# Kernel optimization log

Measured on AMD Instinct MI355X. Metric: run time of the kernel, lower is better.

The kernel has to match this reference:

```python
import jax, jax.numpy as jnp
import numpy as np

N_ROUTES = 200000
N_REGIONS = 2048
D_IN = 3
EMBED_DIM0 = 100
LSTM_DIM = 100
H1 = 1000
D_OUT = 100


def setup_inputs() -> dict:
    key = jax.random.key(0)
    ks = jax.random.split(key, 14)
    s = 0.1
    return {
        "routes_last": jax.random.normal(ks[0], (N_ROUTES, D_IN), jnp.float32),
        "route_region_ids": jax.random.randint(ks[1], (N_ROUTES,), 0, N_REGIONS),
        # linear0: Linear(3, 100)
        "W0": jax.random.normal(ks[2], (EMBED_DIM0, D_IN), jnp.float32) * s,
        "b0": jax.random.normal(ks[3], (EMBED_DIM0,), jnp.float32) * s,
        # LSTMCell(100, 100): gate order i, f, g, o
        "Wih": jax.random.normal(ks[4], (4 * LSTM_DIM, EMBED_DIM0), jnp.float32) * s,
        "bih": jax.random.normal(ks[5], (4 * LSTM_DIM,), jnp.float32) * s,
        "Whh": jax.random.normal(ks[6], (4 * LSTM_DIM, LSTM_DIM), jnp.float32) * s,
        "bhh": jax.random.normal(ks[7], (4 * LSTM_DIM,), jnp.float32) * s,
        # learned initial state (nn.Parameter rand(1, lstm_dim))
        "h0": jax.random.uniform(ks[8], (1, LSTM_DIM), jnp.float32),
        "c0": jax.random.uniform(ks[9], (1, LSTM_DIM), jnp.float32),
        # linears1: Linear(100,1000) -> ReLU -> Linear(1000,100)
        "W1": jax.random.normal(ks[10], (H1, LSTM_DIM), jnp.float32) * s,
        "b1": jax.random.normal(ks[11], (H1,), jnp.float32) * s,
        "W2": jax.random.normal(ks[12], (D_OUT, H1), jnp.float32) * s,
        "b2": jax.random.normal(ks[13], (D_OUT,), jnp.float32) * s,
        "num_regions": N_REGIONS,
    }


def reference(routes_last, route_region_ids, W0, b0, Wih, bih, Whh, bhh, h0, c0, W1, b1, W2, b2, num_regions):
    # Note: the original LSTM loop always restarts from (h0, c0) and keeps only the
    # last hx, so only the last timestep of each route matters. routes_last is that point.
    e = routes_last @ W0.T + b0                       # [N, 100]
    gates = e @ Wih.T + bih + (h0 @ Whh.T + bhh)      # [N, 400]; h0 broadcasts
    i_g, f_g, g_g, o_g = jnp.split(gates, 4, axis=-1)
    c = jax.nn.sigmoid(f_g) * c0 + jax.nn.sigmoid(i_g) * jnp.tanh(g_g)
    h = jax.nn.sigmoid(o_g) * jnp.tanh(c)             # [N, 100]
    hx = jax.nn.relu(h @ W1.T + b1) @ W2.T + b2       # [N, 100]
    # sum routes within each region (ragged sum)
    region_emb = jax.ops.segment_sum(hx, route_region_ids, num_segments=num_regions)  # [R, 100]
    region_emb = region_emb / jnp.linalg.norm(region_emb, axis=-1, keepdims=True)
    cov = region_emb @ region_emb.T                   # [R, R] cosine similarity
    idx = jnp.arange(num_regions)
    cov = cov.at[idx, idx].set(-jnp.inf)
    return cov
```

## Files before the change

### kernel.cpp

```cpp
#include <hip/hip_runtime.h>
#include <math.h>

#define NR 200000
#define NREG 2048
#define BR 128
#define NBLK 1563

typedef short bf16x8 __attribute__((ext_vector_type(8)));
typedef float f32x4 __attribute__((ext_vector_type(4)));

#define SH_WIH 410752
#define SH_W1  (SH_WIH + 57344)
#define SH_W2  (SH_W1 + 131072)
#define B_LIST 1427712
#define B_CNT  2227712
#define B_BASE 2235904
#define B_CURS 2244112
#define B_HXB  2252800
#define WS_REQ 91852800ULL

#define L_SA  0
#define L_SB  16384
#define L_HB  30720
#define L_T1  63488
#define L_B1C 79872
#define L_RID 80128
#define L_BYTES 80640
#define A_XS  (L_T1)
#define A_GBP (L_T1 + 1536)
#define A_C0P (L_T1 + 3328)

__device__ __forceinline__ unsigned f2bf(float f) {
    unsigned u = __builtin_bit_cast(unsigned, f);
    u += 0x7fff + ((u >> 16) & 1);
    return u >> 16;
}
__device__ __forceinline__ float sigm(float x) { return 1.0f / (1.0f + __expf(-x)); }
__device__ __forceinline__ float tanhfast(float x) {
    float t = __expf(2.0f * fabsf(x));
    float r = 1.0f - 2.0f / (t + 1.0f);
    return copysignf(r, x);
}
__device__ __forceinline__ f32x4 mfma16(bf16x8 a, bf16x8 b, f32x4 c) {
    return __builtin_amdgcn_mfma_f32_16x16x32_bf16(a, b, c, 0, 0, 0);
}

__global__ __launch_bounds__(1024) void k_zero(float* __restrict__ p, int n) {
    int i = blockIdx.x * 1024 + threadIdx.x;
    if (i < n) p[i] = 0.0f;
}

__global__ __launch_bounds__(256) void k_hist(const int* __restrict__ ids,
                                              int* __restrict__ cnt) {
    int i = blockIdx.x * 256 + threadIdx.x;
    if (i < NR) atomicAdd(&cnt[ids[i]], 1);
}

__global__ __launch_bounds__(1024) void k_scan(const int* __restrict__ cnt,
                                               int* __restrict__ base,
                                               int* __restrict__ cursor) {
    __shared__ int sc[2048];
    const int t = threadIdx.x;
    sc[t] = cnt[t];
    sc[t + 1024] = cnt[t + 1024];
    __syncthreads();
    for (int off = 1; off < 2048; off <<= 1) {
        int v0 = (t >= off) ? sc[t - off] : 0;
        int v1 = sc[t + 1024 - off];
        __syncthreads();
        sc[t] += v0;
        sc[t + 1024] += v1;
        __syncthreads();
    }
    int b0 = (t == 0) ? 0 : sc[t - 1];
    int b1v = sc[t + 1023];
    base[t] = b0;          cursor[t] = b0;
    base[t + 1024] = b1v;  cursor[t + 1024] = b1v;
    if (t == 0) base[2048] = sc[2047];
}

__global__ __launch_bounds__(256) void k_scatter(const int* __restrict__ ids,
                                                 int* __restrict__ cursor,
                                                 int* __restrict__ list) {
    int i = blockIdx.x * 256 + threadIdx.x;
    if (i < NR) {
        int pos = atomicAdd(&cursor[ids[i]], 1);
        list[pos] = i;
    }
}

__global__ __launch_bounds__(256) void k_prep(
    const float* __restrict__ Wih, const float* __restrict__ bih,
    const float* __restrict__ bhh, const float* __restrict__ Whh,
    const float* __restrict__ h0,  const float* __restrict__ c0,
    const float* __restrict__ W1,  const float* __restrict__ W2,
    float* __restrict__ wsf, short* __restrict__ wsh)
{
    int idx = blockIdx.x * 256 + threadIdx.x;
    if (idx < 57344) {
        int st = idx >> 13, s = idx & 8191;
        int row = s >> 7, c4 = (s >> 3) & 15, e = s & 7;
        int kc = c4 ^ (row & 15);
        int k = kc * 8 + e;
        int g = row >> 4, j = st * 16 + (row & 15);
        float v = (j < 100 && k < 100) ? Wih[(g * 100 + j) * 100 + k] : 0.f;
        wsh[SH_WIH + idx] = (short)f2bf(v);
        return;
    }
    idx -= 57344;
    if (idx < 131072) {
        int st = idx >> 13, s = idx & 8191;
        int row = s >> 7, c4 = (s >> 3) & 15, e = s & 7;
        int kc = c4 ^ (row & 15);
        int k = kc * 8 + e;
        int m = st * 64 + row;
        float v = (m < 1000 && k < 100) ? W1[m * 100 + k] : 0.f;
        wsh[SH_W1 + idx] = (short)f2bf(v);
        return;
    }
    idx -= 131072;
    if (idx < 114688) {
        int st = idx / 7168, s = idx - st * 7168;
        int row = s >> 6, c4 = (s >> 3) & 7, e = s & 7;
        int kc = c4 ^ (row & 7);
        int m = st * 64 + kc * 8 + e;
        float v = (row < 100 && m < 1000) ? W2[row * 1000 + m] : 0.f;
        wsh[SH_W2 + idx] = (short)f2bf(v);
        return;
    }
    idx -= 114688;
    if (idx < 448) {
        int jt = idx >> 6, r = idx & 63, g = r >> 4, j = jt * 16 + (r & 15);
        float s = 0.f;
        if (j < 100) {
            s = bih[g * 100 + j] + bhh[g * 100 + j];
            const float* wr = &Whh[(g * 100 + j) * 100];
            for (int k = 0; k < 100; ++k) s += h0[k] * wr[k];
        }
        wsf[204800 + idx] = s;
        return;
    }
    idx -= 448;
    if (idx < 112) wsf[205248 + idx] = (idx < 100) ? c0[idx] : 0.f;
}

__global__ __launch_bounds__(256, 2) void k_routes(
    const float* __restrict__ routes, const int* __restrict__ ids,
    const float* __restrict__ W0, const float* __restrict__ b0,
    const float* __restrict__ b1, const float* __restrict__ b2,
    const float* __restrict__ wsf, const short* __restrict__ wsh,
    float* __restrict__ racc, float* __restrict__ hxb, int use_hxb)
{
    __shared__ __align__(16) float ldsf[L_BYTES / 4];
    char* L = (char*)ldsf;
    const int tid = threadIdx.x;
    const int w = tid >> 6, l = tid & 63;
    const int lr = l & 15, lg = l >> 4;
    const int rbase = blockIdx.x * BR;

    float* xs  = (float*)(L + A_XS);
    float* gbp = (float*)(L + A_GBP);
    float* c0p = (float*)(L + A_C0P);
    float* b1c = (float*)(L + L_B1C);
    int*   rid = (int*)(L + L_RID);

    if (tid < 96) {
        float4 v;
        int gi = rbase * 3 + tid * 4;
        v.x = (gi + 0 < NR * 3) ? routes[gi + 0] : 0.f;
        v.y = (gi + 1 < NR * 3) ? routes[gi + 1] : 0.f;
        v.z = (gi + 2 < NR * 3) ? routes[gi + 2] : 0.f;
        v.w = (gi + 3 < NR * 3) ? routes[gi + 3] : 0.f;
        *(float4*)(xs + tid * 4) = v;
    } else if (tid >= 128) {
        int t = tid - 128;
        rid[t] = (rbase + t < NR) ? ids[rbase + t] : 0;
    }
    for (int i = tid; i < 448; i += 256) gbp[i] = wsf[204800 + i];
    for (int i = tid; i < 112; i += 256) c0p[i] = wsf[205248 + i];
    if (tid < 128) {
        int q = tid & 15;
        f32x4 z = {0.f, 0.f, 0.f, 0.f};
        *(f32x4*)(L + L_HB + tid * 256 + ((14 ^ q) << 4)) = z;
        *(f32x4*)(L + L_HB + tid * 256 + ((15 ^ q) << 4)) = z;
    }
    __syncthreads();

    bf16x8 be[2][4];
    #pragma unroll
    for (int rt = 0; rt < 2; ++rt) {
        int rl = w * 32 + rt * 16 + lr;
        float x0 = xs[rl * 3], x1 = xs[rl * 3 + 1], x2 = xs[rl * 3 + 2];
        #pragma unroll
        for (int ks = 0; ks < 4; ++ks) {
            bf16x8 v;
            #pragma unroll
            for (int j = 0; j < 8; ++j) {
                int k = ks * 32 + lg * 8 + j;
                float e = 0.f;
                if (k < 100)
                    e = b0[k] + x0 * W0[3 * k] + x1 * W0[3 * k + 1] + x2 * W0[3 * k + 2];
                v[j] = (short)f2bf(e);
            }
            be[rt][ks] = v;
        }
    }

    const f32x4* gsrc = (const f32x4*)(wsh + SH_WIH);
    f32x4 pa[4];
    #pragma unroll
    for (int t = 0; t < 4; ++t) pa[t] = gsrc[tid + t * 256];
    #pragma unroll 1
    for (int jt = 0; jt < 7; ++jt) {
        __syncthreads();
        {
            f32x4* dst = (f32x4*)(L + L_SA);
            #pragma unroll
            for (int t = 0; t < 4; ++t) dst[tid + t * 256] = pa[t];
        }
        __syncthreads();
        if (jt < 6) {
            #pragma unroll
            for (int t = 0; t < 4; ++t) pa[t] = gsrc[(jt + 1) * 1024 + tid + t * 256];
        }
        f32x4 acc[4][2];
        #pragma unroll
        for (int g = 0; g < 4; ++g) {
            bf16x8 aw[4];
            #pragma unroll
            for (int ks = 0; ks < 4; ++ks)
                aw[ks] = *(bf16x8*)(L + L_SA + (g * 16 + lr) * 256 + (((lg + 4 * ks) ^ lr) << 4));
            #pragma unroll
            for (int rt = 0; rt < 2; ++rt) {
                f32x4 a = {0.f, 0.f, 0.f, 0.f};
                #pragma unroll
                for (int ks = 0; ks < 4; ++ks) a = mfma16(aw[ks], be[rt][ks], a);
                acc[g][rt] = a;
            }
        }
        const f32x4 gi_ = *(const f32x4*)(gbp + jt * 64 +  0 + lg * 4);
        const f32x4 gf_ = *(const f32x4*)(gbp + jt * 64 + 16 + lg * 4);
        const f32x4 gg_ = *(const f32x4*)(gbp + jt * 64 + 32 + lg * 4);
        const f32x4 go_ = *(const f32x4*)(gbp + jt * 64 + 48 + lg * 4);
        const f32x4 c0v = *(const f32x4*)(c0p + jt * 16 + lg * 4);
        #pragma unroll
        for (int rt = 0; rt < 2; ++rt) {
            int route = w * 32 + rt * 16 + lr;
            short4 hs;
            #pragma unroll
            for (int i = 0; i < 4; ++i) {
                float iv = sigm(acc[0][rt][i] + gi_[i]);
                float fv = sigm(acc[1][rt][i] + gf_[i]);
                float gv = tanhfast(acc[2][rt][i] + gg_[i]);
                float ov = sigm(acc[3][rt][i] + go_[i]);
                float c  = fv * c0v[i] + iv * gv;
                float h  = ov * tanhfast(c);
                ((short*)&hs)[i] = (short)f2bf(h);
            }
            int c4 = 2 * jt + (lg >> 1);
            *(short4*)(L + L_HB + route * 256 + ((c4 ^ lr) << 4) + (lg & 1) * 8) = hs;
        }
    }

    bf16x8 bh[2][4];
    #pragma unroll
    for (int rt = 0; rt < 2; ++rt)
        #pragma unroll
        for (int ks = 0; ks < 4; ++ks)
            bh[rt][ks] = *(bf16x8*)(L + L_HB + (w * 32 + rt * 16 + lr) * 256 + (((lg + 4 * ks) ^ lr) << 4));

    const f32x4* s1 = (const f32x4*)(wsh + SH_W1);
    const f32x4* s2 = (const f32x4*)(wsh + SH_W2);
    f32x4 p1[4], p2[4];
    float pb1 = 0.f;
    #pragma unroll
    for (int t = 0; t < 4; ++t) p1[t] = s1[tid + t * 256];
    #pragma unroll
    for (int t = 0; t < 4; ++t) {
        int s = tid + t * 256;
        p2[t] = (s < 896) ? s2[s] : f32x4{0.f, 0.f, 0.f, 0.f};
    }
    if (tid < 64) pb1 = b1[tid];

    f32x4 hx[7][2] = {};
    #pragma unroll 1
    for (int mc = 0; mc < 16; ++mc) {
        __syncthreads();
        {
            f32x4* d1 = (f32x4*)(L + L_SA);
            #pragma unroll
            for (int t = 0; t < 4; ++t) d1[tid + t * 256] = p1[t];
            f32x4* d2 = (f32x4*)(L + L_SB);
            #pragma unroll
            for (int t = 0; t < 4; ++t) {
                int s = tid + t * 256;
                if (s < 896) d2[s] = p2[t];
            }
            if (tid < 64) b1c[tid] = pb1;
        }
        __syncthreads();
        if (mc < 15) {
            #pragma unroll
            for (int t = 0; t < 4; ++t) p1[t] = s1[(mc + 1) * 1024 + tid + t * 256];
            #pragma unroll
            for (int t = 0; t < 4; ++t) {
                int s = tid + t * 256;
                if (s < 896) p2[t] = s2[(mc + 1) * 896 + s];
            }
            if (tid < 64) {
                int m = (mc + 1) * 64 + tid;
                pb1 = (m < 1000) ? b1[m] : 0.f;
            }
        }
        #pragma unroll
        for (int mt = 0; mt < 4; ++mt) {
            bf16x8 aw[4];
            #pragma unroll
            for (int ks = 0; ks < 4; ++ks)
                aw[ks] = *(bf16x8*)(L + L_SA + (mt * 16 + lr) * 256 + (((lg + 4 * ks) ^ lr) << 4));
            const f32x4 b1v = *(const f32x4*)(b1c + mt * 16 + lg * 4);
            #pragma unroll
            for (int rt = 0; rt < 2; ++rt) {
                f32x4 a = {0.f, 0.f, 0.f, 0.f};
                #pragma unroll
                for (int ks = 0; ks < 4; ++ks) a = mfma16(aw[ks], bh[rt][ks], a);
                int route = w * 32 + rt * 16 + lr;
                short4 ts;
                #pragma unroll
                for (int i = 0; i < 4; ++i)
                    ((short*)&ts)[i] = (short)f2bf(fmaxf(a[i] + b1v[i], 0.f));
                int c4 = 2 * mt + (lg >> 1);
                *(short4*)(L + L_T1 + route * 128 + ((c4 ^ (lr & 7)) << 4) + (lg & 1) * 8) = ts;
            }
        }
        bf16x8 bt[2][2];
        #pragma unroll
        for (int rt = 0; rt < 2; ++rt)
            #pragma unroll
            for (int k2 = 0; k2 < 2; ++k2)
                bt[rt][k2] = *(bf16x8*)(L + L_T1 + (w * 32 + rt * 16 + lr) * 128 + (((4 * k2 + lg) ^ (lr & 7)) << 4));
        #pragma unroll
        for (int dt = 0; dt < 7; ++dt) {
            bf16x8 aw2[2];
            #pragma unroll
            for (int k2 = 0; k2 < 2; ++k2)
                aw2[k2] = *(bf16x8*)(L + L_SB + (dt * 16 + lr) * 128 + (((4 * k2 + lg) ^ (lr & 7)) << 4));
            #pragma unroll
            for (int rt = 0; rt < 2; ++rt)
                #pragma unroll
                for (int k2 = 0; k2 < 2; ++k2)
                    hx[dt][rt] = mfma16(aw2[k2], bt[rt][k2], hx[dt][rt]);
        }
    }

    if (use_hxb) {
        #pragma unroll
        for (int rt = 0; rt < 2; ++rt) {
            int rl = w * 32 + rt * 16 + lr;
            if (rbase + rl < NR) {
                float* dst = hxb + (rbase + rl) * 112;
                #pragma unroll
                for (int dt = 0; dt < 7; ++dt) {
                    int d0 = dt * 16 + lg * 4;
                    f32x4 v = hx[dt][rt];
                    #pragma unroll
                    for (int i = 0; i < 4; ++i)
                        v[i] += (d0 + i < 100) ? b2[d0 + i] : 0.f;
                    *(f32x4*)(dst + d0) = v;
                }
            }
        }
    } else {
        #pragma unroll
        for (int rt = 0; rt < 2; ++rt) {
            int rl = w * 32 + rt * 16 + lr;
            if (rbase + rl < NR) {
                float* dst = &racc[rid[rl] * 100];
                #pragma unroll
                for (int dt = 0; dt < 7; ++dt) {
                    int dbase = dt * 16 + lg * 4;
                    #pragma unroll
                    for (int i = 0; i < 4; ++i) {
                        int d = dbase + i;
                        if (d < 100) atomicAdd(&dst[d], hx[dt][rt][i] + b2[d]);
                    }
                }
            }
        }
    }
}

__global__ __launch_bounds__(128) void k_segsum(const int* __restrict__ base,
                                                const int* __restrict__ list,
                                                const float* __restrict__ hxb,
                                                float* __restrict__ racc) {
    __shared__ int ll[1024];
    __shared__ float pp[2];
    const int reg = blockIdx.x, t = threadIdx.x;
    const int s = base[reg], e = base[reg + 1];
    const int n = e - s;
    const int d = t;
    float acc = 0.f;
    if (n <= 1024) {
        for (int i = t; i < n; i += 128) ll[i] = list[s + i];
        __syncthreads();
        #pragma unroll 2
        for (int i = 0; i < n; ++i) {
            int rt = ll[i];
            if (d < 112) acc += hxb[rt * 112 + d];
        }
    } else {
        for (int i = 0; i < n; ++i) {
            int rt = list[s + i];
            if (d < 112) acc += hxb[rt * 112 + d];
        }
    }
    float sq = (d < 100) ? acc * acc : 0.f;
    #pragma unroll
    for (int o = 32; o; o >>= 1) sq += __shfl_xor(sq, o);
    if ((t & 63) == 0) pp[t >> 6] = sq;
    __syncthreads();
    float rn = 1.0f / sqrtf(pp[0] + pp[1]);
    if (d < 100) racc[reg * 100 + d] = acc * rn;
}

__global__ __launch_bounds__(64) void k_norm(float* __restrict__ E) {
    const int r = blockIdx.x;
    const int l = threadIdx.x;
    float v0 = E[r * 100 + l];
    float v1 = (l < 36) ? E[r * 100 + 64 + l] : 0.0f;
    float s = v0 * v0 + v1 * v1;
    #pragma unroll
    for (int o = 32; o; o >>= 1) s += __shfl_xor(s, o);
    const float rn = 1.0f / sqrtf(s);
    E[r * 100 + l] = v0 * rn;
    if (l < 36) E[r * 100 + 64 + l] = v1 * rn;
}

#define ST 68
__global__ __launch_bounds__(256) void k_cov(const float* __restrict__ E,
                                             float* __restrict__ out) {
    __shared__ float aT[100 * ST];
    __shared__ float bT[100 * ST];
    const int bi = blockIdx.x, bj = blockIdx.y;
    const int tid = threadIdx.x;
    for (int idx = tid; idx < 6400; idx += 256) {
        int ii = idx / 100, k = idx - ii * 100;
        aT[k * ST + ii] = E[(bi * 64 + ii) * 100 + k];
        bT[k * ST + ii] = E[(bj * 64 + ii) * 100 + k];
    }
    __syncthreads();
    const int rg = tid >> 4, jg = tid & 15;
    const int r0 = rg * 4, c0 = jg * 4;
    float acc[4][4] = {};
    #pragma unroll 4
    for (int k = 0; k < 100; ++k) {
        const float4 a = *(const float4*)&aT[k * ST + r0];
        const float4 b = *(const float4*)&bT[k * ST + c0];
        const float ar[4] = {a.x, a.y, a.z, a.w};
        const float br[4] = {b.x, b.y, b.z, b.w};
        #pragma unroll
        for (int i = 0; i < 4; ++i)
            #pragma unroll
            for (int jj = 0; jj < 4; ++jj)
                acc[i][jj] += ar[i] * br[jj];
    }
    const float dsent = -3.0e38f;
    #pragma unroll
    for (int i = 0; i < 4; ++i) {
        const int row = bi * 64 + r0 + i;
        const int colb = bj * 64 + c0;
        float4 v;
        v.x = (row == colb + 0) ? dsent : acc[i][0];
        v.y = (row == colb + 1) ? dsent : acc[i][1];
        v.z = (row == colb + 2) ? dsent : acc[i][2];
        v.w = (row == colb + 3) ? dsent : acc[i][3];
        *(float4*)&out[row * 2048 + colb] = v;
    }
}

extern "C" void kernel_launch(void* const* d_in, const int* in_sizes, int n_in,
                              void* d_out, int out_size, void* d_ws, size_t ws_size,
                              hipStream_t stream) {
    (void)in_sizes; (void)n_in; (void)out_size;
    const float* routes = (const float*)d_in[0];
    const int*   ids    = (const int*)d_in[1];
    const float* W0  = (const float*)d_in[2];
    const float* b0  = (const float*)d_in[3];
    const float* Wih = (const float*)d_in[4];
    const float* bih = (const float*)d_in[5];
    const float* Whh = (const float*)d_in[6];
    const float* bhh = (const float*)d_in[7];
    const float* h0  = (const float*)d_in[8];
    const float* c0  = (const float*)d_in[9];
    const float* W1  = (const float*)d_in[10];
    const float* b1  = (const float*)d_in[11];
    const float* W2  = (const float*)d_in[12];
    const float* b2  = (const float*)d_in[13];
    float* out  = (float*)d_out;
    float* wsf  = (float*)d_ws;
    short* wsh  = (short*)d_ws;
    char*  wsb  = (char*)d_ws;
    float* racc = wsf;
    int*   list = (int*)(wsb + B_LIST);
    int*   cnt  = (int*)(wsb + B_CNT);
    int*   base = (int*)(wsb + B_BASE);
    int*   curs = (int*)(wsb + B_CURS);
    float* hxb  = (float*)(wsb + B_HXB);

    const bool fast = (ws_size >= WS_REQ);

    hipLaunchKernelGGL(k_prep, dim3(1187), dim3(256), 0, stream,
                       Wih, bih, bhh, Whh, h0, c0, W1, W2, wsf, wsh);
    if (fast) {
        hipLaunchKernelGGL(k_zero, dim3(2), dim3(1024), 0, stream, (float*)cnt, 2048);
        hipLaunchKernelGGL(k_hist, dim3(782), dim3(256), 0, stream, ids, cnt);
        hipLaunchKernelGGL(k_scan, dim3(1), dim3(1024), 0, stream, cnt, base, curs);
        hipLaunchKernelGGL(k_scatter, dim3(782), dim3(256), 0, stream, ids, curs, list);
        hipLaunchKernelGGL(k_routes, dim3(NBLK), dim3(256), 0, stream,
                           routes, ids, W0, b0, b1, b2, wsf, wsh, racc, hxb, 1);
        hipLaunchKernelGGL(k_segsum, dim3(NREG), dim3(128), 0, stream,
                           base, list, hxb, racc);
    } else {
        hipLaunchKernelGGL(k_zero, dim3(200), dim3(1024), 0, stream, racc, 204800);
        hipLaunchKernelGGL(k_routes, dim3(NBLK), dim3(256), 0, stream,
                           routes, ids, W0, b0, b1, b2, wsf, wsh, racc, hxb, 0);
        hipLaunchKernelGGL(k_norm, dim3(NREG), dim3(64), 0, stream, racc);
    }
    hipLaunchKernelGGL(k_cov, dim3(32, 32), dim3(256), 0, stream, racc, out);
}
```

Before: 400.6 us.

## Shrink LDS footprint to fit three blocks per CU and use packed bf16 converts

```diff
diff --git a/kernel.cpp b/kernel.cpp
--- a/kernel.cpp
+++ b/kernel.cpp
@@ -20,20 +20,25 @@
 #define WS_REQ 91852800ULL
 
 #define L_SA  0
+#define L_HB  16384
 #define L_SB  16384
-#define L_HB  30720
-#define L_T1  63488
-#define L_B1C 79872
-#define L_RID 80128
-#define L_BYTES 80640
-#define A_XS  (L_T1)
-#define A_GBP (L_T1 + 1536)
-#define A_C0P (L_T1 + 3328)
+#define L_T1  30720
+#define L_XS  49152
+#define L_GBP 50688
+#define L_C0P 52480
+#define L_B1C 52928
+#define L_RID 53184
+#define L_BYTES 53696
 
 __device__ __forceinline__ unsigned f2bf(float f) {
     unsigned u = __builtin_bit_cast(unsigned, f);
     u += 0x7fff + ((u >> 16) & 1);
     return u >> 16;
+}
+__device__ __forceinline__ unsigned cvtpk(float lo, float hi) {
+    unsigned r;
+    asm("v_cvt_pk_bf16_f32 %0, %1, %2" : "=v"(r) : "v"(lo), "v"(hi));
+    return r;
 }
 __device__ __forceinline__ float sigm(float x) { return 1.0f / (1.0f + __expf(-x)); }
 __device__ __forceinline__ float tanhfast(float x) {
@@ -144,7 +149,7 @@
     if (idx < 112) wsf[205248 + idx] = (idx < 100) ? c0[idx] : 0.f;
 }
 
-__global__ __launch_bounds__(256, 2) void k_routes(
+__global__ __launch_bounds__(256, 3) void k_routes(
     const float* __restrict__ routes, const int* __restrict__ ids,
     const float* __restrict__ W0, const float* __restrict__ b0,
     const float* __restrict__ b1, const float* __restrict__ b2,
@@ -158,9 +163,9 @@
     const int lr = l & 15, lg = l >> 4;
     const int rbase = blockIdx.x * BR;
 
-    float* xs  = (float*)(L + A_XS);
-    float* gbp = (float*)(L + A_GBP);
-    float* c0p = (float*)(L + A_C0P);
+    float* xs  = (float*)(L + L_XS);
+    float* gbp = (float*)(L + L_GBP);
+    float* c0p = (float*)(L + L_C0P);
     float* b1c = (float*)(L + L_B1C);
     int*   rid = (int*)(L + L_RID);
 
@@ -246,7 +251,7 @@
         #pragma unroll
         for (int rt = 0; rt < 2; ++rt) {
             int route = w * 32 + rt * 16 + lr;
-            short4 hs;
+            float hv[4];
             #pragma unroll
             for (int i = 0; i < 4; ++i) {
                 float iv = sigm(acc[0][rt][i] + gi_[i]);
@@ -254,11 +259,13 @@
                 float gv = tanhfast(acc[2][rt][i] + gg_[i]);
                 float ov = sigm(acc[3][rt][i] + go_[i]);
                 float c  = fv * c0v[i] + iv * gv;
-                float h  = ov * tanhfast(c);
-                ((short*)&hs)[i] = (short)f2bf(h);
-            }
+                hv[i] = ov * tanhfast(c);
+            }
+            uint2 hu;
+            hu.x = cvtpk(hv[0], hv[1]);
+            hu.y = cvtpk(hv[2], hv[3]);
             int c4 = 2 * jt + (lg >> 1);
-            *(short4*)(L + L_HB + route * 256 + ((c4 ^ lr) << 4) + (lg & 1) * 8) = hs;
+            *(uint2*)(L + L_HB + route * 256 + ((c4 ^ lr) << 4) + (lg & 1) * 8) = hu;
         }
     }
 
@@ -325,12 +332,11 @@
                 #pragma unroll
                 for (int ks = 0; ks < 4; ++ks) a = mfma16(aw[ks], bh[rt][ks], a);
                 int route = w * 32 + rt * 16 + lr;
-                short4 ts;
-                #pragma unroll
-                for (int i = 0; i < 4; ++i)
-                    ((short*)&ts)[i] = (short)f2bf(fmaxf(a[i] + b1v[i], 0.f));
+                uint2 tu;
+                tu.x = cvtpk(fmaxf(a[0] + b1v[0], 0.f), fmaxf(a[1] + b1v[1], 0.f));
+                tu.y = cvtpk(fmaxf(a[2] + b1v[2], 0.f), fmaxf(a[3] + b1v[3], 0.f));
                 int c4 = 2 * mt + (lg >> 1);
-                *(short4*)(L + L_T1 + route * 128 + ((c4 ^ (lr & 7)) << 4) + (lg & 1) * 8) = ts;
+                *(uint2*)(L + L_T1 + route * 128 + ((c4 ^ (lr & 7)) << 4) + (lg & 1) * 8) = tu;
             }
         }
         bf16x8 bt[2][2];
```

Measured after the change: 406.3 us. Within noise of the previous version (+1.4%).
